# Kernel tuning notes

Hardware: AMD Instinct MI355X
Metric: run time of the kernel (lower is better)

Reference implementation:

```python
import jax, jax.numpy as jnp
import numpy as np

B, CIN, H, W = 256, 1280, 7, 7
A, NCLS, HID, NGT = 9, 20, 128, 40
OUT_DIM = 5 * A + NCLS  # 65


def setup_inputs() -> dict:
    key = jax.random.key(0)
    ks = jax.random.split(key, 8)
    features = jax.random.normal(ks[0], (B, CIN, H, W), jnp.float32)
    # grid: (x, y) centers of each feature cell, in feature-map coordinates
    grid = jax.random.uniform(ks[1], (B, H, W, 2), jnp.float32) * 7.0
    # GT boxes (x1, y1, x2, y2, class), padded count NGT per image
    xy1 = jax.random.uniform(ks[2], (B, NGT, 2), jnp.float32) * 5.0
    wh = jax.random.uniform(ks[3], (B, NGT, 2), jnp.float32) * 2.0 + 0.5
    cls = jax.random.randint(ks[4], (B, NGT, 1), 0, NCLS).astype(jnp.float32)
    bboxes = jnp.concatenate([xy1, xy1 + wh, cls], axis=-1)
    # anchor shapes (w, h) as in SingleStageDetector.__init__
    anc = jnp.array([[1.0, 1], [2, 2], [3, 3], [4, 4], [5, 5],
                     [2, 3], [3, 2], [3, 5], [5, 3]], jnp.float32)
    W1 = jax.random.normal(ks[5], (HID, CIN), jnp.float32) * 0.02
    b1 = jnp.zeros((HID,), jnp.float32)
    W2 = jax.random.normal(ks[6], (OUT_DIM, HID), jnp.float32) * 0.02
    b2 = jnp.zeros((OUT_DIM,), jnp.float32)
    return dict(features=features, grid=grid, bboxes=bboxes, anc=anc,
                W1=W1, b1=b1, W2=W2, b2=b2)


def reference(features, grid, bboxes, anc, W1, b1, W2, b2):
    Bx = features.shape[0]
    # --- PredictionNetwork (inference mode; dropout is identity at eval) ---
    h = jnp.einsum('bchw,oc->bohw', features, W1) + b1[None, :, None, None]
    h = jax.nn.leaky_relu(h, negative_slope=0.01)
    out = jnp.einsum('bchw,oc->bohw', h, W2) + b2[None, :, None, None]
    conf_scores = jax.nn.sigmoid(out[:, 4 * A:5 * A])          # (B, A, H, W)
    offsets = out[:, :4 * A].reshape(Bx, A, 4, H, W)
    offsets = jnp.concatenate(
        [jax.nn.sigmoid(offsets[:, :, :2]) - 0.5, offsets[:, :, 2:]], axis=2)
    class_scores = out[:, 5 * A:]                               # (B, C, H, W)
    # --- GenerateAnchor: (B, A, H, W, 4) as (x_tl, y_tl, x_br, y_br) ---
    ctr = grid[:, None]                    # (B, 1, H, W, 2)
    half = anc[None, :, None, None, :] / 2  # (1, A, 1, 1, 2)
    anchors = jnp.concatenate([ctr - half, ctr + half], axis=-1)
    # --- IoU: (B, A*H*W, N) ---
    P = anchors.reshape(Bx, -1, 4)          # (B, AHW, 4)
    gt = bboxes[..., :4]                    # (B, N, 4)
    tl = jnp.maximum(P[:, :, None, :2], gt[:, None, :, :2])
    br = jnp.minimum(P[:, :, None, 2:], gt[:, None, :, 2:])
    inter = jnp.prod(jnp.clip(br - tl, 0.0), axis=-1)  # (B, AHW, N)
    # torch code zeroes intersections for proposals with any coord <= 0
    legal = (jnp.min(P, axis=-1) > 0)[..., None]
    inter = inter * legal
    p_area = ((P[:, :, 2] - P[:, :, 0]) * (P[:, :, 3] - P[:, :, 1]))[:, :, None]
    g_area = ((gt[:, :, 2] - gt[:, :, 0]) * (gt[:, :, 3] - gt[:, :, 1]))[:, None, :]
    iou_mat = inter / (g_area + p_area - inter)
    return (conf_scores, offsets, class_scores, iou_mat)
```

## Files before the change

### kernel.cpp

```cpp
#include <hip/hip_runtime.h>


#define CIN_  1280
#define HW_   49
#define HID_  128
#define OUTD_ 65
#define NGT_  40
#define NP_   441

#define CONF_OFF 0
#define OFFS_OFF 112896
#define CLS_OFF  564480
#define IOU_OFF  815360

#define WS_W1F_U32 81920u
#define WS_W2F_U32 5120u

#define CHUNK_DW 12544

typedef __bf16 bf16x8 __attribute__((ext_vector_type(8)));
typedef float  f32x4  __attribute__((ext_vector_type(4)));

__device__ __forceinline__ unsigned pack2bf(float lo, float hi) {
    unsigned short a = __builtin_bit_cast(unsigned short, (__bf16)lo);
    unsigned short b = __builtin_bit_cast(unsigned short, (__bf16)hi);
    return (unsigned)a | ((unsigned)b << 16);
}
__device__ __forceinline__ float sigmoidf_(float v) { return 1.f / (1.f + __expf(-v)); }

__device__ __forceinline__ bf16x8 ld_frag(const unsigned* p) {
    union { uint4 u; bf16x8 v; } x;
    x.u = *(const uint4*)p;
    return x.v;
}
__device__ __forceinline__ bf16x8 as_bf(uint4 u) {
    union { uint4 u; bf16x8 v; } x; x.u = u; return x.v;
}
__device__ __forceinline__ bf16x8 frag_from_f32(const float* p) {
    union { unsigned u[4]; bf16x8 v; } x;
    #pragma unroll
    for (int j = 0; j < 4; ++j)
        x.u[j] = pack2bf(p[(2 * j) * 49], p[(2 * j + 1) * 49]);
    return x.v;
}
__device__ __forceinline__ void gload_lds16(const float* g, unsigned* l) {
    __builtin_amdgcn_global_load_lds(
        (const __attribute__((address_space(1))) unsigned*)g,
        (__attribute__((address_space(3))) unsigned*)l, 16, 0, 0);
}

__global__ __launch_bounds__(256) void prep_w(
    const float* __restrict__ W1, const float* __restrict__ W2,
    unsigned* __restrict__ ws)
{
    int X = blockIdx.x * 256 + threadIdx.x;
    if (X < (int)WS_W1F_U32) {
        int sub = X & 3, lane = (X >> 2) & 63, f = X >> 8;
        int mt = f & 7, K32 = f >> 3;
        int o = mt * 16 + (lane & 15);
        int c = K32 * 32 + (lane >> 4) * 8 + sub * 2;
        float2 v = *(const float2*)(W1 + o * CIN_ + c);
        ws[X] = pack2bf(v.x, v.y);
    } else {
        int Y = X - (int)WS_W1F_U32;
        int sub = Y & 3, lane = (Y >> 2) & 63, f = Y >> 8;
        int mt2 = f % 5, ks2 = f / 5;
        int o2 = mt2 * 16 + (lane & 15);
        int c = ks2 * 32 + (lane >> 4) * 8 + sub * 2;
        unsigned val = 0;
        if (o2 < OUTD_) {
            float2 v = *(const float2*)(W2 + o2 * HID_ + c);
            val = pack2bf(v.x, v.y);
        }
        ws[WS_W1F_U32 + Y] = val;
    }
}

__global__ __launch_bounds__(512, 2) void fused_main(
    const float* __restrict__ F,
    const float* __restrict__ grd,
    const float* __restrict__ bbox,
    const float* __restrict__ anc,
    const unsigned* __restrict__ wsW,
    const float* __restrict__ B1,
    const float* __restrict__ B2,
    float* __restrict__ out)
{
    __shared__ __align__(16) unsigned lds[2 * CHUNK_DW + 64];
    unsigned* smHT = lds;

    const int tid  = threadIdx.x;
    const int b    = blockIdx.x;
    const int lane = tid & 63;
    const int w    = tid >> 6;
    const int wo   = w >> 1;
    const int wh   = w & 1;
    const int quad = lane >> 4;
    const int m16  = lane & 15;

    const float* Fb = F + b * (CIN_ * HW_);

    #define STAGE(c)                                                         \
        {                                                                    \
            const float* srcb = Fb + (c) * CHUNK_DW;                         \
            unsigned*    dstb = lds + (((c) & 1) ? CHUNK_DW : 0);            \
            _Pragma("unroll")                                                \
            for (int i = 0; i < 6; ++i) {                                    \
                int s0 = w * 1536 + i * 256;                                 \
                gload_lds16(srcb + s0 + lane * 4, dstb + s0);                \
            }                                                                \
            if (w == 7) gload_lds16(srcb + 12288 + lane * 4, dstb + 12288);  \
        }

    STAGE(0);
    __syncthreads();

    const uint4* Af = (const uint4*)wsW;
    f32x4 acc[2][2] = {{(f32x4)(0.f), (f32x4)(0.f)}, {(f32x4)(0.f), (f32x4)(0.f)}};

    #pragma unroll
    for (int c = 0; c < 5; ++c) {
        uint4 Ar[8][2];
        #pragma unroll
        for (int kk = 0; kk < 8; ++kk) {
            #pragma unroll
            for (int mo = 0; mo < 2; ++mo)
                Ar[kk][mo] = Af[(((c * 8 + kk) * 8) + (wo * 2 + mo)) * 64 + lane];
        }
        __builtin_amdgcn_sched_barrier(0);
        if (c < 4) STAGE(c + 1);
        __builtin_amdgcn_sched_barrier(0);

        const float* fb = (const float*)(lds + ((c & 1) ? CHUNK_DW : 0));
        #pragma unroll
        for (int kk = 0; kk < 8; ++kk) {
            bf16x8 A0 = as_bf(Ar[kk][0]);
            bf16x8 A1 = as_bf(Ar[kk][1]);
            #pragma unroll
            for (int nh = 0; nh < 2; ++nh) {
                const float* pb = fb + (kk * 32 + quad * 8) * 49
                                     + (wh * 32 + nh * 16 + m16);
                bf16x8 Bf = frag_from_f32(pb);
                acc[0][nh] = __builtin_amdgcn_mfma_f32_16x16x32_bf16(A0, Bf, acc[0][nh], 0, 0, 0);
                acc[1][nh] = __builtin_amdgcn_mfma_f32_16x16x32_bf16(A1, Bf, acc[1][nh], 0, 0, 0);
            }
        }
        __builtin_amdgcn_sched_barrier(0);
        __syncthreads();
    }

    #pragma unroll
    for (int mo = 0; mo < 2; ++mo) {
        #pragma unroll
        for (int nh = 0; nh < 2; ++nh) {
            int row = (wh * 2 + nh) * 16 + m16;
            #pragma unroll
            for (int rp = 0; rp < 2; ++rp) {
                int o0 = (wo * 2 + mo) * 16 + quad * 4 + 2 * rp;
                float v0 = acc[mo][nh][2 * rp]     + B1[o0];
                float v1 = acc[mo][nh][2 * rp + 1] + B1[o0 + 1];
                v0 = v0 > 0.f ? v0 : 0.01f * v0;
                v1 = v1 > 0.f ? v1 : 0.01f * v1;
                smHT[row * 68 + (o0 >> 1)] = pack2bf(v0, v1);
            }
        }
    }
    __syncthreads();

    for (int T = w; T < 20; T += 8) {
        int m2 = T % 5, nt2 = T / 5;
        const uint4* A2p = (const uint4*)(wsW + WS_W1F_U32) + m2 * 64 + lane;
        uint4 a20 = A2p[0], a21 = A2p[320], a22 = A2p[640], a23 = A2p[960];
        f32x4 c2 = (f32x4)(0.f);
        const unsigned* Bb = smHT + (nt2 * 16 + m16) * 68 + quad * 4;
        c2 = __builtin_amdgcn_mfma_f32_16x16x32_bf16(as_bf(a20), ld_frag(Bb +  0), c2, 0, 0, 0);
        c2 = __builtin_amdgcn_mfma_f32_16x16x32_bf16(as_bf(a21), ld_frag(Bb + 16), c2, 0, 0, 0);
        c2 = __builtin_amdgcn_mfma_f32_16x16x32_bf16(as_bf(a22), ld_frag(Bb + 32), c2, 0, 0, 0);
        c2 = __builtin_amdgcn_mfma_f32_16x16x32_bf16(as_bf(a23), ld_frag(Bb + 48), c2, 0, 0, 0);
        int hw = nt2 * 16 + m16;
        if (hw < HW_) {
            #pragma unroll
            for (int r = 0; r < 4; ++r) {
                int o2 = m2 * 16 + quad * 4 + r;
                if (o2 >= OUTD_) continue;
                float aa = c2[r] + B2[o2];
                unsigned dst; float val;
                if (o2 < 36) {
                    int an9 = o2 >> 2, kk = o2 & 3;
                    val = (kk < 2) ? (sigmoidf_(aa) - 0.5f) : aa;
                    dst = OFFS_OFF + b * 1764 + an9 * 196 + kk * 49 + hw;
                } else if (o2 < 45) {
                    val = sigmoidf_(aa);
                    dst = CONF_OFF + b * 441 + (o2 - 36) * 49 + hw;
                } else {
                    val = aa;
                    dst = CLS_OFF + b * 980 + (o2 - 45) * 49 + hw;
                }
                out[dst] = val;
            }
        }
    }

    {
        int gl = (lane < NGT_) ? lane : 0;
        const float* gb = bbox + b * 200 + gl * 5;
        float gx1 = gb[0], gy1 = gb[1], gx2 = gb[2], gy2 = gb[3];
        float gA = (gx2 - gx1) * (gy2 - gy1);
        #pragma unroll 4
        for (int p = w; p < NP_; p += 8) {
            int a9 = p / 49, r = p - a9 * 49;
            float2 ct = *(const float2*)(grd + b * 98 + 2 * r);
            float hx = anc[2 * a9] * 0.5f,  hy = anc[2 * a9 + 1] * 0.5f;
            float px1 = ct.x - hx, py1 = ct.y - hy, px2 = ct.x + hx, py2 = ct.y + hy;
            float pA = (px2 - px1) * (py2 - py1);
            float legal = (fminf(fminf(px1, py1), fminf(px2, py2)) > 0.f) ? 1.f : 0.f;
            float tlx = fmaxf(px1, gx1), tly = fmaxf(py1, gy1);
            float brx = fminf(px2, gx2), bry = fminf(py2, gy2);
            float dx = fmaxf(brx - tlx, 0.f), dy = fmaxf(bry - tly, 0.f);
            float inter = dx * dy * legal;
            float iou = __fdividef(inter, gA + pA - inter);
            if (lane < NGT_)
                out[IOU_OFF + b * (NP_ * NGT_) + p * 40 + lane] = iou;
        }
    }
}

extern "C" void kernel_launch(void* const* d_in, const int* in_sizes, int n_in,
                              void* d_out, int out_size, void* d_ws, size_t ws_size,
                              hipStream_t stream) {
    const float* F  = (const float*)d_in[0];
    const float* G  = (const float*)d_in[1];
    const float* BB = (const float*)d_in[2];
    const float* AN = (const float*)d_in[3];
    const float* W1 = (const float*)d_in[4];
    const float* B1 = (const float*)d_in[5];
    const float* W2 = (const float*)d_in[6];
    const float* B2 = (const float*)d_in[7];
    float* out = (float*)d_out;
    unsigned* wsu = (unsigned*)d_ws;

    prep_w<<<340, 256, 0, stream>>>(W1, W2, wsu);
    fused_main<<<256, 512, 0, stream>>>(F, G, BB, AN, wsu, B1, B2, out);
}
```

Baseline: 132.4 us.

## Split each image across two blocks and load features directly into registers

The grid doubles to 512 blocks of 256 threads, so each block handles half of the 49 spatial columns (32 or 17 of them) for one image. The LDS double-buffered global_load_lds staging of feature chunks is gone. Each wave now loads its fp32 feature values and weight fragments straight into registers, software-pipelined one K-step ahead. The aim is more blocks in flight per CU and less LDS and barrier traffic, at the cost of strided, uncoalesced global loads, clamped duplicate column reads in the second half, and W1 fragments fetched by both blocks of each image.

```diff
diff --git a/kernel.cpp b/kernel.cpp
--- a/kernel.cpp
+++ b/kernel.cpp
@@ -16,8 +16,6 @@
 #define WS_W1F_U32 81920u
 #define WS_W2F_U32 5120u
 
-#define CHUNK_DW 12544
-
 typedef __bf16 bf16x8 __attribute__((ext_vector_type(8)));
 typedef float  f32x4  __attribute__((ext_vector_type(4)));
 
@@ -36,17 +34,11 @@
 __device__ __forceinline__ bf16x8 as_bf(uint4 u) {
     union { uint4 u; bf16x8 v; } x; x.u = u; return x.v;
 }
-__device__ __forceinline__ bf16x8 frag_from_f32(const float* p) {
-    union { unsigned u[4]; bf16x8 v; } x;
+__device__ __forceinline__ bf16x8 pack8(const float* v) {
+    union { unsigned u[4]; bf16x8 x; } r;
     #pragma unroll
-    for (int j = 0; j < 4; ++j)
-        x.u[j] = pack2bf(p[(2 * j) * 49], p[(2 * j + 1) * 49]);
-    return x.v;
-}
-__device__ __forceinline__ void gload_lds16(const float* g, unsigned* l) {
-    __builtin_amdgcn_global_load_lds(
-        (const __attribute__((address_space(1))) unsigned*)g,
-        (__attribute__((address_space(3))) unsigned*)l, 16, 0, 0);
+    for (int j = 0; j < 4; ++j) r.u[j] = pack2bf(v[2 * j], v[2 * j + 1]);
+    return r.x;
 }
 
 __global__ __launch_bounds__(256) void prep_w(
@@ -76,7 +68,7 @@
     }
 }
 
-__global__ __launch_bounds__(512, 2) void fused_main(
+__global__ __launch_bounds__(256, 4) void fused_main(
     const float* __restrict__ F,
     const float* __restrict__ grd,
     const float* __restrict__ bbox,
@@ -86,77 +78,66 @@
     const float* __restrict__ B2,
     float* __restrict__ out)
 {
-    __shared__ __align__(16) unsigned lds[2 * CHUNK_DW + 64];
-    unsigned* smHT = lds;
+    __shared__ __align__(16) unsigned smHT[32 * 68];
 
     const int tid  = threadIdx.x;
-    const int b    = blockIdx.x;
+    const int id   = blockIdx.x;
+    const int half = id >> 8;
+    const int b    = id & 255;
     const int lane = tid & 63;
     const int w    = tid >> 6;
-    const int wo   = w >> 1;
-    const int wh   = w & 1;
     const int quad = lane >> 4;
     const int m16  = lane & 15;
+    const int hw0  = half * 32;
 
     const float* Fb = F + b * (CIN_ * HW_);
-
-    #define STAGE(c)                                                         \
+    const int colA = hw0 + m16;
+    const int colB = min(hw0 + 16 + m16, HW_ - 1);
+    const int mt0 = 2 * w, mt1 = 2 * w + 1;
+    const uint4* Af = (const uint4*)wsW;
+
+    #define LOADK(k, vA, vB, ra0, ra1)                                       \
         {                                                                    \
-            const float* srcb = Fb + (c) * CHUNK_DW;                         \
-            unsigned*    dstb = lds + (((c) & 1) ? CHUNK_DW : 0);            \
+            const float* pk = Fb + ((k) * 32 + quad * 8) * 49;               \
             _Pragma("unroll")                                                \
-            for (int i = 0; i < 6; ++i) {                                    \
-                int s0 = w * 1536 + i * 256;                                 \
-                gload_lds16(srcb + s0 + lane * 4, dstb + s0);                \
+            for (int j = 0; j < 8; ++j) {                                    \
+                vA[j] = pk[j * 49 + colA];                                   \
+                vB[j] = pk[j * 49 + colB];                                   \
             }                                                                \
-            if (w == 7) gload_lds16(srcb + 12288 + lane * 4, dstb + 12288);  \
-        }
-
-    STAGE(0);
-    __syncthreads();
-
-    const uint4* Af = (const uint4*)wsW;
+            ra0 = Af[((k) * 8 + mt0) * 64 + lane];                           \
+            ra1 = Af[((k) * 8 + mt1) * 64 + lane];                           \
+        }
+
     f32x4 acc[2][2] = {{(f32x4)(0.f), (f32x4)(0.f)}, {(f32x4)(0.f), (f32x4)(0.f)}};
-
+    float cA[8], cB[8]; uint4 ca0, ca1;
+    LOADK(0, cA, cB, ca0, ca1);
     #pragma unroll
-    for (int c = 0; c < 5; ++c) {
-        uint4 Ar[8][2];
-        #pragma unroll
-        for (int kk = 0; kk < 8; ++kk) {
+    for (int k = 0; k < 40; ++k) {
+        float nA[8], nB[8]; uint4 na0, na1;
+        if (k < 39) LOADK(k + 1, nA, nB, na0, na1);
+        bf16x8 Bf0 = pack8(cA);
+        bf16x8 Bf1 = pack8(cB);
+        bf16x8 A0 = as_bf(ca0);
+        bf16x8 A1 = as_bf(ca1);
+        acc[0][0] = __builtin_amdgcn_mfma_f32_16x16x32_bf16(A0, Bf0, acc[0][0], 0, 0, 0);
+        acc[0][1] = __builtin_amdgcn_mfma_f32_16x16x32_bf16(A0, Bf1, acc[0][1], 0, 0, 0);
+        acc[1][0] = __builtin_amdgcn_mfma_f32_16x16x32_bf16(A1, Bf0, acc[1][0], 0, 0, 0);
+        acc[1][1] = __builtin_amdgcn_mfma_f32_16x16x32_bf16(A1, Bf1, acc[1][1], 0, 0, 0);
+        if (k < 39) {
             #pragma unroll
-            for (int mo = 0; mo < 2; ++mo)
-                Ar[kk][mo] = Af[(((c * 8 + kk) * 8) + (wo * 2 + mo)) * 64 + lane];
-        }
-        __builtin_amdgcn_sched_barrier(0);
-        if (c < 4) STAGE(c + 1);
-        __builtin_amdgcn_sched_barrier(0);
-
-        const float* fb = (const float*)(lds + ((c & 1) ? CHUNK_DW : 0));
-        #pragma unroll
-        for (int kk = 0; kk < 8; ++kk) {
-            bf16x8 A0 = as_bf(Ar[kk][0]);
-            bf16x8 A1 = as_bf(Ar[kk][1]);
-            #pragma unroll
-            for (int nh = 0; nh < 2; ++nh) {
-                const float* pb = fb + (kk * 32 + quad * 8) * 49
-                                     + (wh * 32 + nh * 16 + m16);
-                bf16x8 Bf = frag_from_f32(pb);
-                acc[0][nh] = __builtin_amdgcn_mfma_f32_16x16x32_bf16(A0, Bf, acc[0][nh], 0, 0, 0);
-                acc[1][nh] = __builtin_amdgcn_mfma_f32_16x16x32_bf16(A1, Bf, acc[1][nh], 0, 0, 0);
-            }
-        }
-        __builtin_amdgcn_sched_barrier(0);
-        __syncthreads();
+            for (int j = 0; j < 8; ++j) { cA[j] = nA[j]; cB[j] = nB[j]; }
+            ca0 = na0; ca1 = na1;
+        }
     }
 
     #pragma unroll
     for (int mo = 0; mo < 2; ++mo) {
         #pragma unroll
         for (int nh = 0; nh < 2; ++nh) {
-            int row = (wh * 2 + nh) * 16 + m16;
+            int row = nh * 16 + m16;
             #pragma unroll
             for (int rp = 0; rp < 2; ++rp) {
-                int o0 = (wo * 2 + mo) * 16 + quad * 4 + 2 * rp;
+                int o0 = (2 * w + mo) * 16 + quad * 4 + 2 * rp;
                 float v0 = acc[mo][nh][2 * rp]     + B1[o0];
                 float v1 = acc[mo][nh][2 * rp + 1] + B1[o0 + 1];
                 v0 = v0 > 0.f ? v0 : 0.01f * v0;
@@ -167,7 +148,7 @@
     }
     __syncthreads();
 
-    for (int T = w; T < 20; T += 8) {
+    for (int T = w; T < 10; T += 4) {
         int m2 = T % 5, nt2 = T / 5;
         const uint4* A2p = (const uint4*)(wsW + WS_W1F_U32) + m2 * 64 + lane;
         uint4 a20 = A2p[0], a21 = A2p[320], a22 = A2p[640], a23 = A2p[960];
@@ -177,7 +158,7 @@
         c2 = __builtin_amdgcn_mfma_f32_16x16x32_bf16(as_bf(a21), ld_frag(Bb + 16), c2, 0, 0, 0);
         c2 = __builtin_amdgcn_mfma_f32_16x16x32_bf16(as_bf(a22), ld_frag(Bb + 32), c2, 0, 0, 0);
         c2 = __builtin_amdgcn_mfma_f32_16x16x32_bf16(as_bf(a23), ld_frag(Bb + 48), c2, 0, 0, 0);
-        int hw = nt2 * 16 + m16;
+        int hw = hw0 + nt2 * 16 + m16;
         if (hw < HW_) {
             #pragma unroll
             for (int r = 0; r < 4; ++r) {
@@ -206,8 +187,10 @@
         const float* gb = bbox + b * 200 + gl * 5;
         float gx1 = gb[0], gy1 = gb[1], gx2 = gb[2], gy2 = gb[3];
         float gA = (gx2 - gx1) * (gy2 - gy1);
+        const int pstart = half ? 221 : 0;
+        const int pend   = half ? NP_ : 221;
         #pragma unroll 4
-        for (int p = w; p < NP_; p += 8) {
+        for (int p = pstart + w; p < pend; p += 4) {
             int a9 = p / 49, r = p - a9 * 49;
             float2 ct = *(const float2*)(grd + b * 98 + 2 * r);
             float hx = anc[2 * a9] * 0.5f,  hy = anc[2 * a9 + 1] * 0.5f;
@@ -240,5 +223,5 @@
     unsigned* wsu = (unsigned*)d_ws;
 
     prep_w<<<340, 256, 0, stream>>>(W1, W2, wsu);
-    fused_main<<<256, 512, 0, stream>>>(F, G, BB, AN, wsu, B1, B2, out);
-}
+    fused_main<<<512, 256, 0, stream>>>(F, G, BB, AN, wsu, B1, B2, out);
+}
```

Result: slower. 146.4 us (+10.5%).

## Split first GEMM over K into four blocks per image with last-block reduction

Applied to the files above, without the earlier changes.

The first 1x1 conv is split along the 1280-channel dimension into four slices, so there are 1024 blocks instead of 256. Each block converts its slice to bf16 in LDS and writes fp32 partial sums to workspace. An atomic counter picks the last block per image, which sums the partials, applies bias and leaky ReLU, and runs the rest of the pipeline. The goal is to fill more compute units on the GPU and shrink LDS use so more blocks fit per CU. The cost is extra global traffic for the partials, a threadfence/atomic handshake, and the loss of the old asynchronous double-buffered staging.

```diff
diff --git a/kernel.cpp b/kernel.cpp
--- a/kernel.cpp
+++ b/kernel.cpp
@@ -15,8 +15,10 @@
 
 #define WS_W1F_U32 81920u
 #define WS_W2F_U32 5120u
-
-#define CHUNK_DW 12544
+#define HP_OFF     87040u
+#define HP_KQ      (128u*52u)
+#define HP_IMG     (4u*HP_KQ)
+#define DONE_OFF   (HP_OFF + 256u*HP_IMG)
 
 typedef __bf16 bf16x8 __attribute__((ext_vector_type(8)));
 typedef float  f32x4  __attribute__((ext_vector_type(4)));
@@ -35,18 +37,6 @@
 }
 __device__ __forceinline__ bf16x8 as_bf(uint4 u) {
     union { uint4 u; bf16x8 v; } x; x.u = u; return x.v;
-}
-__device__ __forceinline__ bf16x8 frag_from_f32(const float* p) {
-    union { unsigned u[4]; bf16x8 v; } x;
-    #pragma unroll
-    for (int j = 0; j < 4; ++j)
-        x.u[j] = pack2bf(p[(2 * j) * 49], p[(2 * j + 1) * 49]);
-    return x.v;
-}
-__device__ __forceinline__ void gload_lds16(const float* g, unsigned* l) {
-    __builtin_amdgcn_global_load_lds(
-        (const __attribute__((address_space(1))) unsigned*)g,
-        (__attribute__((address_space(3))) unsigned*)l, 16, 0, 0);
 }
 
 __global__ __launch_bounds__(256) void prep_w(
@@ -54,6 +44,7 @@
     unsigned* __restrict__ ws)
 {
     int X = blockIdx.x * 256 + threadIdx.x;
+    if (X < 256) ws[DONE_OFF + X] = 0u;
     if (X < (int)WS_W1F_U32) {
         int sub = X & 3, lane = (X >> 2) & 63, f = X >> 8;
         int mt = f & 7, K32 = f >> 3;
@@ -76,93 +67,108 @@
     }
 }
 
-__global__ __launch_bounds__(512, 2) void fused_main(
+__global__ __launch_bounds__(512, 6) void fused_main(
     const float* __restrict__ F,
     const float* __restrict__ grd,
     const float* __restrict__ bbox,
     const float* __restrict__ anc,
     const unsigned* __restrict__ wsW,
+    float* __restrict__ wsF,
     const float* __restrict__ B1,
     const float* __restrict__ B2,
     float* __restrict__ out)
 {
-    __shared__ __align__(16) unsigned lds[2 * CHUNK_DW + 64];
-    unsigned* smHT = lds;
+    __shared__ __align__(16) unsigned lds[49 * 164];
+    __shared__ int isLast;
 
     const int tid  = threadIdx.x;
-    const int b    = blockIdx.x;
+    const int id   = blockIdx.x;
+    const int kq   = id >> 8;
+    const int b    = id & 255;
     const int lane = tid & 63;
     const int w    = tid >> 6;
-    const int wo   = w >> 1;
-    const int wh   = w & 1;
     const int quad = lane >> 4;
     const int m16  = lane & 15;
 
-    const float* Fb = F + b * (CIN_ * HW_);
-
-    #define STAGE(c)                                                         \
-        {                                                                    \
-            const float* srcb = Fb + (c) * CHUNK_DW;                         \
-            unsigned*    dstb = lds + (((c) & 1) ? CHUNK_DW : 0);            \
-            _Pragma("unroll")                                                \
-            for (int i = 0; i < 6; ++i) {                                    \
-                int s0 = w * 1536 + i * 256;                                 \
-                gload_lds16(srcb + s0 + lane * 4, dstb + s0);                \
-            }                                                                \
-            if (w == 7) gload_lds16(srcb + 12288 + lane * 4, dstb + 12288);  \
-        }
-
-    STAGE(0);
-    __syncthreads();
-
-    const uint4* Af = (const uint4*)wsW;
-    f32x4 acc[2][2] = {{(f32x4)(0.f), (f32x4)(0.f)}, {(f32x4)(0.f), (f32x4)(0.f)}};
-
-    #pragma unroll
-    for (int c = 0; c < 5; ++c) {
-        uint4 Ar[8][2];
+    const float* Fsl = F + b * (CIN_ * HW_) + kq * 15680;
+    #pragma unroll
+    for (int it = 0; it < 16; ++it) {
+        int i = it * 512 + tid;
+        if (i < 7840) {
+            int cp = i / 49, col = i - cp * 49;
+            float v0 = Fsl[cp * 98 + col];
+            float v1 = Fsl[cp * 98 + 49 + col];
+            lds[col * 164 + cp] = pack2bf(v0, v1);
+        }
+    }
+    __syncthreads();
+
+    const uint4* AFs = (const uint4*)wsW + (kq * 80 + w) * 64 + lane;
+    int colc[4];
+    #pragma unroll
+    for (int nt = 0; nt < 4; ++nt) {
+        int c = nt * 16 + m16;
+        colc[nt] = (c < HW_ ? c : HW_ - 1) * 164 + quad * 4;
+    }
+    f32x4 acc[4] = {(f32x4)(0.f), (f32x4)(0.f), (f32x4)(0.f), (f32x4)(0.f)};
+    uint4 a0 = AFs[0], a1 = AFs[512];
+    #pragma unroll
+    for (int k = 0; k < 10; ++k) {
+        uint4 an = AFs[(k < 8 ? k + 2 : 9) * 512];
+        bf16x8 A = as_bf(a0);
         #pragma unroll
-        for (int kk = 0; kk < 8; ++kk) {
+        for (int nt = 0; nt < 4; ++nt) {
+            bf16x8 Bf = ld_frag(lds + colc[nt] + k * 16);
+            acc[nt] = __builtin_amdgcn_mfma_f32_16x16x32_bf16(A, Bf, acc[nt], 0, 0, 0);
+        }
+        a0 = a1; a1 = an;
+    }
+
+    {
+        float* hp = wsF + HP_OFF + (unsigned)(b * 4 + kq) * HP_KQ;
+        #pragma unroll
+        for (int nt = 0; nt < 4; ++nt) {
+            int col = nt * 16 + m16;
+            if (col < HW_) {
+                #pragma unroll
+                for (int r = 0; r < 4; ++r) {
+                    int o = w * 16 + quad * 4 + r;
+                    hp[o * 52 + col] = acc[nt][r];
+                }
+            }
+        }
+    }
+
+    __threadfence();
+    __syncthreads();
+    if (tid == 0) {
+        unsigned old = atomicAdd((unsigned*)wsF + DONE_OFF + b, 1u);
+        isLast = (old == 3u);
+    }
+    __syncthreads();
+    if (!isLast) return;
+    __threadfence();
+
+    unsigned* smHT = lds;
+    for (int i = tid; i < 15 * 68; i += 512)
+        smHT[(49 + i / 68) * 68 + (i % 68)] = 0u;
+    const float* hpb = wsF + HP_OFF + (unsigned)b * HP_IMG;
+    #pragma unroll
+    for (int it = 0; it < 7; ++it) {
+        int i = it * 512 + tid;
+        if (i < 3136) {
+            int op = i / 49, col = i - op * 49;
+            int o0 = 2 * op;
+            float s0 = 0.f, s1 = 0.f;
             #pragma unroll
-            for (int mo = 0; mo < 2; ++mo)
-                Ar[kk][mo] = Af[(((c * 8 + kk) * 8) + (wo * 2 + mo)) * 64 + lane];
-        }
-        __builtin_amdgcn_sched_barrier(0);
-        if (c < 4) STAGE(c + 1);
-        __builtin_amdgcn_sched_barrier(0);
-
-        const float* fb = (const float*)(lds + ((c & 1) ? CHUNK_DW : 0));
-        #pragma unroll
-        for (int kk = 0; kk < 8; ++kk) {
-            bf16x8 A0 = as_bf(Ar[kk][0]);
-            bf16x8 A1 = as_bf(Ar[kk][1]);
-            #pragma unroll
-            for (int nh = 0; nh < 2; ++nh) {
-                const float* pb = fb + (kk * 32 + quad * 8) * 49
-                                     + (wh * 32 + nh * 16 + m16);
-                bf16x8 Bf = frag_from_f32(pb);
-                acc[0][nh] = __builtin_amdgcn_mfma_f32_16x16x32_bf16(A0, Bf, acc[0][nh], 0, 0, 0);
-                acc[1][nh] = __builtin_amdgcn_mfma_f32_16x16x32_bf16(A1, Bf, acc[1][nh], 0, 0, 0);
+            for (int q2 = 0; q2 < 4; ++q2) {
+                s0 += hpb[q2 * HP_KQ + (o0    ) * 52 + col];
+                s1 += hpb[q2 * HP_KQ + (o0 + 1) * 52 + col];
             }
-        }
-        __builtin_amdgcn_sched_barrier(0);
-        __syncthreads();
-    }
-
-    #pragma unroll
-    for (int mo = 0; mo < 2; ++mo) {
-        #pragma unroll
-        for (int nh = 0; nh < 2; ++nh) {
-            int row = (wh * 2 + nh) * 16 + m16;
-            #pragma unroll
-            for (int rp = 0; rp < 2; ++rp) {
-                int o0 = (wo * 2 + mo) * 16 + quad * 4 + 2 * rp;
-                float v0 = acc[mo][nh][2 * rp]     + B1[o0];
-                float v1 = acc[mo][nh][2 * rp + 1] + B1[o0 + 1];
-                v0 = v0 > 0.f ? v0 : 0.01f * v0;
-                v1 = v1 > 0.f ? v1 : 0.01f * v1;
-                smHT[row * 68 + (o0 >> 1)] = pack2bf(v0, v1);
-            }
+            s0 += B1[o0]; s1 += B1[o0 + 1];
+            s0 = s0 > 0.f ? s0 : 0.01f * s0;
+            s1 = s1 > 0.f ? s1 : 0.01f * s1;
+            smHT[col * 68 + op] = pack2bf(s0, s1);
         }
     }
     __syncthreads();
@@ -240,5 +246,6 @@
     unsigned* wsu = (unsigned*)d_ws;
 
     prep_w<<<340, 256, 0, stream>>>(W1, W2, wsu);
-    fused_main<<<256, 512, 0, stream>>>(F, G, BB, AN, wsu, B1, B2, out);
-}
+    fused_main<<<1024, 512, 0, stream>>>(F, G, BB, AN, wsu, (float*)d_ws,
+                                         B1, B2, out);
+}
```

New measurement: 495.8 us. 274% more time.
